# Optimization experiments

Measured on AMD Instinct MI355X. Metric: run time of the kernel, lower is better.

Reference implementation:

```python
import jax, jax.numpy as jnp
import numpy as np

B, N_SPINS, D_MODEL, K_MC = 256, 128, 768, 25


def setup_inputs() -> dict:
    key = jax.random.key(0)
    k1, k2, k3 = jax.random.split(key, 3)
    features = jax.random.normal(k1, (B, N_SPINS, D_MODEL), dtype=jnp.float32)
    coalitions = jax.random.randint(k2, (K_MC, N_SPINS), 0, 2, dtype=jnp.int32)
    w_v = jax.random.normal(k3, (D_MODEL, D_MODEL), dtype=jnp.float32) * 0.02
    scale = jnp.full((1,), 0.1, dtype=jnp.float32)
    return {"features": features, "coalitions": coalitions, "w_v": w_v, "scale": scale}


def reference(features, coalitions, w_v, scale):
    # features: [B, n, d]; coalitions: [K, n] in {0,1}; w_v: [d, d]; scale: [1]
    c = coalitions.astype(features.dtype)                      # [K, n]
    # coalition_value batched over all K coalitions at once:
    # sum_j mask[k,j] * features[b,j,:]  (sum and linear proj commute)
    s = jnp.einsum('kn,bnd->bkd', c, features)                 # [B, K, d]
    proj = s @ w_v                                             # [B, K, d]
    norm = jnp.linalg.norm(proj, axis=-1)                      # [B, K]
    cv = jax.nn.relu(norm * scale[0])                          # coalition values [B, K]
    # Shapley estimate: mean(v | i in S) - mean(v | i not in S)
    cnt_with = c.sum(axis=0)                                   # [n]
    cnt_without = c.shape[0] - cnt_with
    v_with = (cv @ c) / jnp.maximum(cnt_with, 1.0)             # [B, n]
    v_without = (cv @ (1.0 - c)) / jnp.maximum(cnt_without, 1.0)
    valid = (cnt_with > 0) & (cnt_without > 0)                 # [n]
    shapley = jnp.where(valid, v_with - v_without, 0.0)        # [B, n]
    return shapley
```

## Files before the change

kernel.cpp:

```cpp
#include <hip/hip_runtime.h>
#include <hip/hip_bf16.h>
#include <stdint.h>

#define NB  256
#define NSP 128
#define DM  768
#define KMC 25
#define MROWS (NB*KMC)

#define OFF_S    0u
#define OFF_WT   9830400u
#define OFF_N2   11010048u
#define OFF_COEF 11035648u
#define OFF_CB   11049984u

typedef __attribute__((ext_vector_type(8))) short bf16x8;
typedef __attribute__((ext_vector_type(4))) float f32x4;
typedef __attribute__((ext_vector_type(16))) float f32x16;
typedef unsigned int u32;

#define GLOAD_LDS16(gp, lp) \
  __builtin_amdgcn_global_load_lds((const __attribute__((address_space(1))) u32*)(gp), \
                                   (__attribute__((address_space(3))) u32*)(lp), 16, 0, 0)

#define KA_WAITV_BAR(N) asm volatile("s_waitcnt vmcnt(" #N ")\n\ts_barrier" ::: "memory")
#define KA_BAR()        asm volatile("s_barrier" ::: "memory")

__global__ __launch_bounds__(256) void prep_kernel(const float* __restrict__ wv,
                                                   const int* __restrict__ co,
                                                   char* __restrict__ ws) {
  const int blk = blockIdx.x;
  const int t = threadIdx.x;
  if (blk < 144) {
    __shared__ __hip_bfloat16 lt[64][66];
    const int bi = blk / 12, bj = blk % 12;
    const int k0 = bi * 64, n0 = bj * 64;
    #pragma unroll
    for (int i = 0; i < 16; ++i) {
      int idx = t + i * 256;
      int r = idx >> 6, c = idx & 63;
      lt[c][r] = __float2bfloat16(wv[(size_t)(k0 + r) * DM + n0 + c]);
    }
    __syncthreads();
    __hip_bfloat16* wT = (__hip_bfloat16*)(ws + OFF_WT);
    #pragma unroll
    for (int i = 0; i < 16; ++i) {
      int idx = t + i * 256;
      int r = idx >> 6, c = idx & 63;
      wT[(size_t)(n0 + r) * DM + k0 + c] = lt[r][c];
    }
  } else if (blk == 144) {
    if (t < NSP) {
      const int n = t;
      int cw = 0;
      #pragma unroll
      for (int k = 0; k < KMC; ++k) cw += co[k * NSP + n];
      const int cwo = KMC - cw;
      const bool valid = (cw > 0) && (cwo > 0);
      float* coefT = (float*)(ws + OFF_COEF);
      #pragma unroll
      for (int k = 0; k < 28; ++k) {
        float v = 0.f;
        if (valid && k < KMC) v = co[k * NSP + n] ? (1.f / (float)cw) : (-1.f / (float)cwo);
        coefT[n * 28 + k] = v;
      }
    }
  } else if (blk < 170) {
    int i = (blk - 145) * 256 + t;
    if (i < MROWS) ((float*)(ws + OFF_N2))[i] = 0.f;
  } else {
    int k = blk - 170;
    if (t < NSP) {
      float v = (k < KMC) ? (float)co[k * NSP + t] : 0.f;
      ((__hip_bfloat16*)(ws + OFF_CB))[k * NSP + t] = __float2bfloat16(v);
    }
  }
}

#define KACH (16 * 384)

__global__ __launch_bounds__(256, 2) void kA(const float* __restrict__ f,
                                             const __hip_bfloat16* __restrict__ Cb,
                                             __hip_bfloat16* __restrict__ s) {
  const int b = blockIdx.x;
  const int half = blockIdx.y;
  const int tid = threadIdx.x;
  const int w = tid >> 6;
  const int lane = tid & 63;
  const int l31 = lane & 31, l5 = lane >> 5;

  __shared__ __align__(16) float Fs[3][KACH];

  bf16x8 Af[8];
  #pragma unroll
  for (int ks = 0; ks < 8; ++ks)
    Af[ks] = *(const bf16x8*)(Cb + (size_t)l31 * NSP + ks * 16 + l5 * 8);
  asm volatile("s_waitcnt vmcnt(0)" ::: "memory");

  const float* fb = f + (size_t)b * NSP * DM + half * 384;
  int goff[6];
  #pragma unroll
  for (int q = 0; q < 6; ++q) {
    int e = (w * 6 + q) * 256 + lane * 4;
    int r = e / 384, c = e - r * 384;
    goff[q] = r * DM + c;
  }

  f32x16 ac[3];
  #pragma unroll
  for (int nt = 0; nt < 3; ++nt)
    #pragma unroll
    for (int r = 0; r < 16; ++r) ac[nt][r] = 0.f;

#define KA_ISSUE(ck, bi) { \
    const float* fp_ = fb + (size_t)(ck) * 16 * DM; \
    _Pragma("unroll") for (int q = 0; q < 6; ++q) \
      GLOAD_LDS16(fp_ + goff[q], (char*)&Fs[(bi)][0] + ((w * 6 + q) << 10)); }

#define KA_MFMA(ks, bi) { \
    _Pragma("unroll") for (int nt = 0; nt < 3; ++nt) { \
      bf16x8 Bf; \
      _Pragma("unroll") for (int j = 0; j < 8; ++j) { \
        float v_ = Fs[(bi)][(l5 * 8 + j) * 384 + w * 96 + nt * 32 + l31]; \
        __hip_bfloat16 h_ = __float2bfloat16(v_); \
        Bf[j] = *(short*)&h_; } \
      ac[nt] = __builtin_amdgcn_mfma_f32_32x32x16_bf16(Af[ks], Bf, ac[nt], 0, 0, 0); } }

  KA_ISSUE(0, 0) KA_ISSUE(1, 1) KA_ISSUE(2, 2)
  KA_WAITV_BAR(12);  KA_MFMA(0, 0)  KA_BAR();  KA_ISSUE(3, 0)
  KA_WAITV_BAR(12);  KA_MFMA(1, 1)  KA_BAR();  KA_ISSUE(4, 1)
  KA_WAITV_BAR(12);  KA_MFMA(2, 2)  KA_BAR();  KA_ISSUE(5, 2)
  KA_WAITV_BAR(12);  KA_MFMA(3, 0)  KA_BAR();  KA_ISSUE(6, 0)
  KA_WAITV_BAR(12);  KA_MFMA(4, 1)  KA_BAR();  KA_ISSUE(7, 1)
  KA_WAITV_BAR(12);  KA_MFMA(5, 2)
  KA_WAITV_BAR(6);   KA_MFMA(6, 0)
  KA_WAITV_BAR(0);   KA_MFMA(7, 1)

#undef KA_ISSUE
#undef KA_MFMA

  #pragma unroll
  for (int nt = 0; nt < 3; ++nt) {
    int dcol = half * 384 + w * 96 + nt * 32 + l31;
    #pragma unroll
    for (int r = 0; r < 16; ++r) {
      int row = (r & 3) + 8 * (r >> 2) + 4 * l5;
      if (row < KMC)
        s[((size_t)b * KMC + row) * DM + dcol] = __float2bfloat16(ac[nt][r]);
    }
  }
}

#define BM 64
#define BN 192
#define BK 32
#define NTK 24

__global__ __launch_bounds__(256) void kB(char* __restrict__ ws) {
  const int bid = blockIdx.x;
  const int tm = bid >> 2;
  const int tn = bid & 3;
  const int tid = threadIdx.x;
  const int wid = tid >> 6;
  const int lane = tid & 63;
  const int wm = wid >> 1;
  const int wn = wid & 1;

  const __hip_bfloat16* S  = (const __hip_bfloat16*)(ws + OFF_S);
  const __hip_bfloat16* WT = (const __hip_bfloat16*)(ws + OFF_WT);
  float* norm2 = (float*)(ws + OFF_N2);

  __shared__ __align__(16) char As[2][BM * BK * 2];
  __shared__ __align__(16) char Bs[2][BN * BK * 2];

  const char* gA; char *lAA0, *lAA1;
  {
    int li = wid * 64 + lane;
    int r = li >> 2, sl = li & 3;
    int slx = sl ^ ((r >> 1) & 3);
    gA = (const char*)(S + (size_t)(tm * BM + r) * DM) + slx * 16;
    lAA0 = As[0] + wid * 1024;
    lAA1 = As[1] + wid * 1024;
  }
  const char* gB[3]; char *lB0[3], *lB1[3];
  #pragma unroll
  for (int j = 0; j < 3; ++j) {
    int li = (wid * 3 + j) * 64 + lane;
    int r = li >> 2, sl = li & 3;
    int slx = sl ^ ((r >> 1) & 3);
    gB[j] = (const char*)(WT + (size_t)(tn * BN + r) * DM) + slx * 16;
    lB0[j] = Bs[0] + (wid * 3 + j) * 1024;
    lB1[j] = Bs[1] + (wid * 3 + j) * 1024;
  }

  auto stage = [&](int tk, int bsel) {
    size_t koff = (size_t)tk * (BK * 2);
    GLOAD_LDS16(gA + koff, bsel ? lAA1 : lAA0);
    #pragma unroll
    for (int j = 0; j < 3; ++j) GLOAD_LDS16(gB[j] + koff, bsel ? lB1[j] : lB0[j]);
  };

  f32x4 acc[2][6];
  #pragma unroll
  for (int m = 0; m < 2; ++m)
    #pragma unroll
    for (int n = 0; n < 6; ++n)
      #pragma unroll
      for (int j = 0; j < 4; ++j) acc[m][n][j] = 0.f;

  int offA[2], offB[6];
  #pragma unroll
  for (int m = 0; m < 2; ++m) {
    int r = wm * 32 + m * 16 + (lane & 15);
    int sl = (lane >> 4) ^ ((r >> 1) & 3);
    offA[m] = r * 64 + sl * 16;
  }
  #pragma unroll
  for (int n = 0; n < 6; ++n) {
    int r = wn * 96 + n * 16 + (lane & 15);
    int sl = (lane >> 4) ^ ((r >> 1) & 3);
    offB[n] = r * 64 + sl * 16;
  }

  stage(0, 0);
  for (int tk = 0; tk < NTK; ++tk) {
    int cur = tk & 1;
    __syncthreads();
    if (tk + 1 < NTK) stage(tk + 1, cur ^ 1);
    bf16x8 af[2], bfr[6];
    #pragma unroll
    for (int m = 0; m < 2; ++m) af[m] = *(const bf16x8*)(As[cur] + offA[m]);
    #pragma unroll
    for (int n = 0; n < 6; ++n) bfr[n] = *(const bf16x8*)(Bs[cur] + offB[n]);
    #pragma unroll
    for (int m = 0; m < 2; ++m)
      #pragma unroll
      for (int n = 0; n < 6; ++n)
        acc[m][n] = __builtin_amdgcn_mfma_f32_16x16x32_bf16(af[m], bfr[n], acc[m][n], 0, 0, 0);
  }

  float ps[2][4];
  #pragma unroll
  for (int m = 0; m < 2; ++m)
    #pragma unroll
    for (int i = 0; i < 4; ++i) {
      float v = 0.f;
      #pragma unroll
      for (int n = 0; n < 6; ++n) { float x = acc[m][n][i]; v += x * x; }
      #pragma unroll
      for (int d = 1; d < 16; d <<= 1) v += __shfl_xor(v, d, 64);
      ps[m][i] = v;
    }
  if ((lane & 15) == 0) {
    int g = lane >> 4;
    #pragma unroll
    for (int m = 0; m < 2; ++m)
      #pragma unroll
      for (int i = 0; i < 4; ++i)
        atomicAdd(&norm2[tm * BM + wm * 32 + m * 16 + g * 4 + i], ps[m][i]);
  }
}

__global__ __launch_bounds__(128) void kC(const char* __restrict__ ws,
                                          const float* __restrict__ scale,
                                          float* __restrict__ out) {
  const int b = blockIdx.x, n = threadIdx.x;
  const float* norm2 = (const float*)(ws + OFF_N2);
  const float* coefT = (const float*)(ws + OFF_COEF);
  __shared__ float cvs[32];
  if (n < KMC) {
    float nv = norm2[b * KMC + n];
    cvs[n] = fmaxf(sqrtf(fmaxf(nv, 0.f)) * scale[0], 0.f);
  } else if (n < 32) {
    cvs[n] = 0.f;
  }
  __syncthreads();
  float sum = 0.f;
  #pragma unroll
  for (int k = 0; k < KMC; ++k) sum += cvs[k] * coefT[n * 28 + k];
  out[b * NSP + n] = sum;
}

extern "C" void kernel_launch(void* const* d_in, const int* in_sizes, int n_in,
                              void* d_out, int out_size, void* d_ws, size_t ws_size,
                              hipStream_t stream) {
  const float* features   = (const float*)d_in[0];
  const int*   coalitions = (const int*)d_in[1];
  const float* wv         = (const float*)d_in[2];
  const float* scale      = (const float*)d_in[3];
  char* ws = (char*)d_ws;

  prep_kernel<<<202, 256, 0, stream>>>(wv, coalitions, ws);
  dim3 gaa(NB, 2);
  kA<<<gaa, 256, 0, stream>>>(features, (const __hip_bfloat16*)(ws + OFF_CB),
                              (__hip_bfloat16*)(ws + OFF_S));
  kB<<<400, 256, 0, stream>>>(ws);
  kC<<<NB, 128, 0, stream>>>(ws, scale, (float*)d_out);
}
```

Before: 45.87 us.

## Deepen kB LDS pipeline, replace atomics with partial slices, load coalitions directly

kB's GEMM loop moves from a double-buffered LDS pipeline with a __syncthreads per step to a 4-stage ring. Three tiles are in flight, and explicit vmcnt waits plus barriers pace it. The norm-squared atomics become plain stores into 8 per-column-tile partial buffers, which kC sums, so the zero-init pass is gone. kA now reads int coalitions and converts them to bf16 in registers, so prep no longer writes a bf16 copy. This costs more LDS, which may lower occupancy, and adds a few extra reads in kC.

```diff
diff --git a/kernel.cpp b/kernel.cpp
--- a/kernel.cpp
+++ b/kernel.cpp
@@ -10,9 +10,8 @@
 
 #define OFF_S    0u
 #define OFF_WT   9830400u
-#define OFF_N2   11010048u
-#define OFF_COEF 11035648u
-#define OFF_CB   11049984u
+#define OFF_N2P  11010048u
+#define OFF_COEF 11214848u
 
 typedef __attribute__((ext_vector_type(8))) short bf16x8;
 typedef __attribute__((ext_vector_type(4))) float f32x4;
@@ -25,6 +24,7 @@
 
 #define KA_WAITV_BAR(N) asm volatile("s_waitcnt vmcnt(" #N ")\n\ts_barrier" ::: "memory")
 #define KA_BAR()        asm volatile("s_barrier" ::: "memory")
+#define KB_WAIT_BAR(N)  asm volatile("s_waitcnt vmcnt(" #N ") lgkmcnt(0)\n\ts_barrier" ::: "memory")
 
 __global__ __launch_bounds__(256) void prep_kernel(const float* __restrict__ wv,
                                                    const int* __restrict__ co,
@@ -49,7 +49,7 @@
       int r = idx >> 6, c = idx & 63;
       wT[(size_t)(n0 + r) * DM + k0 + c] = lt[r][c];
     }
-  } else if (blk == 144) {
+  } else {
     if (t < NSP) {
       const int n = t;
       int cw = 0;
@@ -65,22 +65,13 @@
         coefT[n * 28 + k] = v;
       }
     }
-  } else if (blk < 170) {
-    int i = (blk - 145) * 256 + t;
-    if (i < MROWS) ((float*)(ws + OFF_N2))[i] = 0.f;
-  } else {
-    int k = blk - 170;
-    if (t < NSP) {
-      float v = (k < KMC) ? (float)co[k * NSP + t] : 0.f;
-      ((__hip_bfloat16*)(ws + OFF_CB))[k * NSP + t] = __float2bfloat16(v);
-    }
   }
 }
 
 #define KACH (16 * 384)
 
 __global__ __launch_bounds__(256, 2) void kA(const float* __restrict__ f,
-                                             const __hip_bfloat16* __restrict__ Cb,
+                                             const int* __restrict__ co,
                                              __hip_bfloat16* __restrict__ s) {
   const int b = blockIdx.x;
   const int half = blockIdx.y;
@@ -93,8 +84,25 @@
 
   bf16x8 Af[8];
   #pragma unroll
-  for (int ks = 0; ks < 8; ++ks)
-    Af[ks] = *(const bf16x8*)(Cb + (size_t)l31 * NSP + ks * 16 + l5 * 8);
+  for (int ks = 0; ks < 8; ++ks) {
+    if (l31 < KMC) {
+      const int* cp = co + l31 * NSP + ks * 16 + l5 * 8;
+      int4 c0 = *(const int4*)(cp);
+      int4 c1 = *(const int4*)(cp + 4);
+      __hip_bfloat16 h;
+      h = __float2bfloat16((float)c0.x); Af[ks][0] = *(short*)&h;
+      h = __float2bfloat16((float)c0.y); Af[ks][1] = *(short*)&h;
+      h = __float2bfloat16((float)c0.z); Af[ks][2] = *(short*)&h;
+      h = __float2bfloat16((float)c0.w); Af[ks][3] = *(short*)&h;
+      h = __float2bfloat16((float)c1.x); Af[ks][4] = *(short*)&h;
+      h = __float2bfloat16((float)c1.y); Af[ks][5] = *(short*)&h;
+      h = __float2bfloat16((float)c1.z); Af[ks][6] = *(short*)&h;
+      h = __float2bfloat16((float)c1.w); Af[ks][7] = *(short*)&h;
+    } else {
+      #pragma unroll
+      for (int j = 0; j < 8; ++j) Af[ks][j] = 0;
+    }
+  }
   asm volatile("s_waitcnt vmcnt(0)" ::: "memory");
 
   const float* fb = f + (size_t)b * NSP * DM + half * 384;
@@ -168,37 +176,32 @@
 
   const __hip_bfloat16* S  = (const __hip_bfloat16*)(ws + OFF_S);
   const __hip_bfloat16* WT = (const __hip_bfloat16*)(ws + OFF_WT);
-  float* norm2 = (float*)(ws + OFF_N2);
-
-  __shared__ __align__(16) char As[2][BM * BK * 2];
-  __shared__ __align__(16) char Bs[2][BN * BK * 2];
-
-  const char* gA; char *lAA0, *lAA1;
+  float* n2p = (float*)(ws + OFF_N2P);
+
+  __shared__ __align__(16) char As[4][BM * BK * 2];
+  __shared__ __align__(16) char Bs[4][BN * BK * 2];
+
+  const char* gA;
   {
     int li = wid * 64 + lane;
     int r = li >> 2, sl = li & 3;
     int slx = sl ^ ((r >> 1) & 3);
     gA = (const char*)(S + (size_t)(tm * BM + r) * DM) + slx * 16;
-    lAA0 = As[0] + wid * 1024;
-    lAA1 = As[1] + wid * 1024;
-  }
-  const char* gB[3]; char *lB0[3], *lB1[3];
+  }
+  const char* gB[3];
   #pragma unroll
   for (int j = 0; j < 3; ++j) {
     int li = (wid * 3 + j) * 64 + lane;
     int r = li >> 2, sl = li & 3;
     int slx = sl ^ ((r >> 1) & 3);
     gB[j] = (const char*)(WT + (size_t)(tn * BN + r) * DM) + slx * 16;
-    lB0[j] = Bs[0] + (wid * 3 + j) * 1024;
-    lB1[j] = Bs[1] + (wid * 3 + j) * 1024;
-  }
-
-  auto stage = [&](int tk, int bsel) {
-    size_t koff = (size_t)tk * (BK * 2);
-    GLOAD_LDS16(gA + koff, bsel ? lAA1 : lAA0);
-    #pragma unroll
-    for (int j = 0; j < 3; ++j) GLOAD_LDS16(gB[j] + koff, bsel ? lB1[j] : lB0[j]);
-  };
+  }
+
+#define KB_STAGE(tk, bi) { \
+    size_t koff_ = (size_t)(tk) * (BK * 2); \
+    GLOAD_LDS16(gA + koff_, As[bi] + wid * 1024); \
+    _Pragma("unroll") for (int j = 0; j < 3; ++j) \
+      GLOAD_LDS16(gB[j] + koff_, Bs[bi] + (wid * 3 + j) * 1024); }
 
   f32x4 acc[2][6];
   #pragma unroll
@@ -222,22 +225,30 @@
     offB[n] = r * 64 + sl * 16;
   }
 
-  stage(0, 0);
-  for (int tk = 0; tk < NTK; ++tk) {
-    int cur = tk & 1;
-    __syncthreads();
-    if (tk + 1 < NTK) stage(tk + 1, cur ^ 1);
-    bf16x8 af[2], bfr[6];
-    #pragma unroll
-    for (int m = 0; m < 2; ++m) af[m] = *(const bf16x8*)(As[cur] + offA[m]);
-    #pragma unroll
-    for (int n = 0; n < 6; ++n) bfr[n] = *(const bf16x8*)(Bs[cur] + offB[n]);
-    #pragma unroll
-    for (int m = 0; m < 2; ++m)
-      #pragma unroll
-      for (int n = 0; n < 6; ++n)
-        acc[m][n] = __builtin_amdgcn_mfma_f32_16x16x32_bf16(af[m], bfr[n], acc[m][n], 0, 0, 0);
-  }
+#define KB_MFMA(bi) { \
+    bf16x8 af[2], bfr[6]; \
+    _Pragma("unroll") for (int m = 0; m < 2; ++m) \
+      af[m] = *(const bf16x8*)(As[bi] + offA[m]); \
+    _Pragma("unroll") for (int n = 0; n < 6; ++n) \
+      bfr[n] = *(const bf16x8*)(Bs[bi] + offB[n]); \
+    _Pragma("unroll") for (int m = 0; m < 2; ++m) \
+      _Pragma("unroll") for (int n = 0; n < 6; ++n) \
+        acc[m][n] = __builtin_amdgcn_mfma_f32_16x16x32_bf16(af[m], bfr[n], acc[m][n], 0, 0, 0); }
+
+  asm volatile("s_waitcnt vmcnt(0)" ::: "memory");
+  KB_STAGE(0, 0) KB_STAGE(1, 1) KB_STAGE(2, 2)
+  #pragma unroll
+  for (int tk = 0; tk < 21; ++tk) {
+    KB_WAIT_BAR(8);
+    KB_MFMA(tk & 3)
+    KB_STAGE(tk + 3, (tk + 3) & 3)
+  }
+  KB_WAIT_BAR(8);  KB_MFMA(21 & 3)
+  KB_WAIT_BAR(4);  KB_MFMA(22 & 3)
+  KB_WAIT_BAR(0);  KB_MFMA(23 & 3)
+
+#undef KB_STAGE
+#undef KB_MFMA
 
   float ps[2][4];
   #pragma unroll
@@ -253,11 +264,12 @@
     }
   if ((lane & 15) == 0) {
     int g = lane >> 4;
+    float* slice = n2p + (size_t)(tn * 2 + wn) * MROWS;
     #pragma unroll
     for (int m = 0; m < 2; ++m)
       #pragma unroll
       for (int i = 0; i < 4; ++i)
-        atomicAdd(&norm2[tm * BM + wm * 32 + m * 16 + g * 4 + i], ps[m][i]);
+        slice[tm * BM + wm * 32 + m * 16 + g * 4 + i] = ps[m][i];
   }
 }
 
@@ -265,11 +277,13 @@
                                           const float* __restrict__ scale,
                                           float* __restrict__ out) {
   const int b = blockIdx.x, n = threadIdx.x;
-  const float* norm2 = (const float*)(ws + OFF_N2);
+  const float* n2p = (const float*)(ws + OFF_N2P);
   const float* coefT = (const float*)(ws + OFF_COEF);
   __shared__ float cvs[32];
   if (n < KMC) {
-    float nv = norm2[b * KMC + n];
+    float nv = 0.f;
+    #pragma unroll
+    for (int q = 0; q < 8; ++q) nv += n2p[(size_t)q * MROWS + b * KMC + n];
     cvs[n] = fmaxf(sqrtf(fmaxf(nv, 0.f)) * scale[0], 0.f);
   } else if (n < 32) {
     cvs[n] = 0.f;
@@ -290,10 +304,9 @@
   const float* scale      = (const float*)d_in[3];
   char* ws = (char*)d_ws;
 
-  prep_kernel<<<202, 256, 0, stream>>>(wv, coalitions, ws);
+  prep_kernel<<<145, 256, 0, stream>>>(wv, coalitions, ws);
   dim3 gaa(NB, 2);
-  kA<<<gaa, 256, 0, stream>>>(features, (const __hip_bfloat16*)(ws + OFF_CB),
-                              (__hip_bfloat16*)(ws + OFF_S));
+  kA<<<gaa, 256, 0, stream>>>(features, coalitions, (__hip_bfloat16*)(ws + OFF_S));
   kB<<<400, 256, 0, stream>>>(ws);
   kC<<<NB, 128, 0, stream>>>(ws, scale, (float*)d_out);
 }
```

Measured after the change: 48.95 us. 6.7% more time.
